# Kernel tuning notes

Measured on AMD Instinct MI355X. Metric: run time of the kernel, lower is better.

Reference implementation:

```python
import jax, jax.numpy as jnp
import numpy as np

N_NODES = 100000


def gcn_conv(x, edge_index, W, b, num_nodes):
    # PyG GCNConv: h = X W; out = D^-1/2 (A+I) D^-1/2 h + b
    h = x @ W
    src, dst = edge_index[0], edge_index[1]
    loop = jnp.arange(num_nodes, dtype=edge_index.dtype)
    src = jnp.concatenate([src, loop])
    dst = jnp.concatenate([dst, loop])
    ew = jnp.ones(src.shape[0], dtype=x.dtype)  # edge_weight=None -> ones
    deg = jax.ops.segment_sum(ew, dst, num_segments=num_nodes)
    dinv = jnp.where(deg > 0, jax.lax.rsqrt(deg), 0.0)
    norm = dinv[src] * ew * dinv[dst]  # [E+N]
    msg = h[src] * norm[:, None]       # gather + scale
    out = jax.ops.segment_sum(msg, dst, num_segments=num_nodes)
    return out + b


def setup_inputs() -> dict:
    key = jax.random.key(0)
    k1, k2, k3, k4 = jax.random.split(key, 4)
    in_c, hid = 128, 128
    x = jax.random.normal(k1, (N_NODES, in_c), dtype=jnp.float32)
    edge_index = jax.random.randint(k2, (2, 1600000), 0, N_NODES, dtype=jnp.int64)
    s = 1.0 / np.sqrt(in_c)
    W1 = jax.random.uniform(k3, (in_c, hid), jnp.float32, -s, s)
    b1 = jnp.zeros((hid,), jnp.float32)
    W2 = jax.random.uniform(k4, (hid, hid), jnp.float32, -s, s)
    b2 = jnp.zeros((hid,), jnp.float32)
    return {"x": x, "edge_index": edge_index, "W1": W1, "b1": b1, "W2": W2, "b2": b2}


def reference(x, edge_index, W1, b1, W2, b2):
    h1 = jax.nn.relu(gcn_conv(x, edge_index, W1, b1, N_NODES))
    h2 = jax.nn.relu(gcn_conv(h1, edge_index, W2, b2, N_NODES))
    return jnp.concatenate([h1, h2], axis=1)  # [N, 2*hidden]
```

## Files before the change

### kernel.cpp

```cpp
#include <hip/hip_runtime.h>
#include <hip/hip_bf16.h>


#define FEAT 128
#define HW 64

typedef __attribute__((ext_vector_type(8))) short short8;
typedef __attribute__((ext_vector_type(4))) float f32x4;

static __device__ inline unsigned pack_bf16(float a, float b) {
    unsigned ua = __float_as_uint(a), ub = __float_as_uint(b);
    ua = (ua + 0x7fff + ((ua >> 16) & 1)) >> 16;
    ub = (ub + 0x7fff + ((ub >> 16) & 1)) >> 16;
    return (ua & 0xffffu) | (ub << 16);
}

static __device__ inline void split2(float x, unsigned short* hi, unsigned short* lo) {
    unsigned u = __float_as_uint(x);
    unsigned uh = (u + 0x7fff + ((u >> 16) & 1)) & 0xffff0000u;
    *hi = (unsigned short)(uh >> 16);
    float lo_f = x - __uint_as_float(uh);
    unsigned ul = __float_as_uint(lo_f);
    *lo = (unsigned short)((ul + 0x7fff + ((ul >> 16) & 1)) >> 16);
}


__global__ void count_edges_kernel(const int* __restrict__ dst, int E,
                                   int* __restrict__ cnt) {
    int e = blockIdx.x * 256 + threadIdx.x;
    if (e < E) atomicAdd(&cnt[dst[e]], 1);
}

__global__ __launch_bounds__(1024) void scan_block_kernel(
    const int* __restrict__ cnt, int* __restrict__ incl,
    int* __restrict__ bsum, float* __restrict__ dinv, int N) {
    __shared__ int s[1024];
    int tid = threadIdx.x;
    int i = blockIdx.x * 1024 + tid;
    int v = (i < N) ? cnt[i] : 0;
    if (i < N) dinv[i] = rsqrtf((float)(v + 1));
    s[tid] = v;
    __syncthreads();
    for (int off = 1; off < 1024; off <<= 1) {
        int add = (tid >= off) ? s[tid - off] : 0;
        __syncthreads();
        s[tid] += add;
        __syncthreads();
    }
    if (i < N) incl[i] = s[tid];
    if (tid == 1023) bsum[blockIdx.x] = s[1023];
}

__global__ __launch_bounds__(128) void scan_bsum_kernel(int* __restrict__ bsum, int NB) {
    __shared__ int s[128];
    int tid = threadIdx.x;
    int v = (tid < NB) ? bsum[tid] : 0;
    s[tid] = v;
    __syncthreads();
    for (int off = 1; off < 128; off <<= 1) {
        int add = (tid >= off) ? s[tid - off] : 0;
        __syncthreads();
        s[tid] += add;
        __syncthreads();
    }
    if (tid < NB) bsum[tid] = s[tid] - v;
}

__global__ void scan_finalize_kernel(const int* __restrict__ incl,
                                     const int* __restrict__ bsum,
                                     int* __restrict__ rowptr, int N) {
    int i = blockIdx.x * 256 + threadIdx.x;
    if (i < N) rowptr[i + 1] = incl[i] + bsum[i >> 10];
    if (i == 0) rowptr[0] = 0;
}

__global__ void fill_csr_kernel(const int* __restrict__ src, const int* __restrict__ dst,
                                int E, const int* __restrict__ rowptr,
                                int* __restrict__ cur, int* __restrict__ csr_src) {
    int e = blockIdx.x * 256 + threadIdx.x;
    if (e < E) {
        int d = dst[e];
        int pos = atomicAdd(&cur[d], 1);
        csr_src[rowptr[d] + pos] = src[e];
    }
}


__global__ void prep_w_kernel(const float* __restrict__ W,
                              unsigned short* __restrict__ wf_hi,
                              unsigned short* __restrict__ wf_lo) {
    int f = blockIdx.x * 256 + threadIdx.x;
    int j = f & 7, lane = (f >> 3) & 63, t = (f >> 9) & 7, ks = f >> 12;
    int k = ks * 32 + (lane >> 4) * 8 + j;
    int n = t * 16 + (lane & 15);
    unsigned short hi, lo;
    split2(W[k * 128 + n], &hi, &lo);
    wf_hi[f] = hi;
    wf_lo[f] = lo;
}


__global__ __launch_bounds__(256) void gemm_mfma_kernel(const float* __restrict__ X, int ldx,
    const unsigned short* __restrict__ wf_hi, const unsigned short* __restrict__ wf_lo,
    unsigned* __restrict__ H, int M) {
    __shared__ unsigned short xs_hi[64 * 128];
    __shared__ unsigned short xs_lo[64 * 128];
    int tid = threadIdx.x;
    int row0 = blockIdx.x * 64;

#pragma unroll
    for (int i = 0; i < 8; ++i) {
        int idx = tid + i * 256;
        int r = idx >> 5, c4 = (idx & 31) * 4;
        int gr = row0 + r;
        float4 v = make_float4(0.f, 0.f, 0.f, 0.f);
        if (gr < M) v = *(const float4*)(X + (size_t)gr * ldx + c4);
        unsigned short h4[4], l4[4];
        split2(v.x, &h4[0], &l4[0]); split2(v.y, &h4[1], &l4[1]);
        split2(v.z, &h4[2], &l4[2]); split2(v.w, &h4[3], &l4[3]);
        int sidx = r * 128 + (c4 ^ ((r & 7) << 3));
        uint2 ph, pl;
        ph.x = (unsigned)h4[0] | ((unsigned)h4[1] << 16);
        ph.y = (unsigned)h4[2] | ((unsigned)h4[3] << 16);
        pl.x = (unsigned)l4[0] | ((unsigned)l4[1] << 16);
        pl.y = (unsigned)l4[2] | ((unsigned)l4[3] << 16);
        *(uint2*)(xs_hi + sidx) = ph;
        *(uint2*)(xs_lo + sidx) = pl;
    }
    __syncthreads();

    int wave = tid >> 6, lane = tid & 63;
    int arow = wave * 16 + (lane & 15);
    int kgrp = (lane >> 4) * 8;

    f32x4 acc[8];
#pragma unroll
    for (int t = 0; t < 8; ++t) acc[t] = (f32x4){0.f, 0.f, 0.f, 0.f};

#pragma unroll
    for (int ks = 0; ks < 4; ++ks) {
        int k0 = ks * 32 + kgrp;
        int aidx = arow * 128 + (k0 ^ ((arow & 7) << 3));
        short8 a_hi = *(const short8*)(xs_hi + aidx);
        short8 a_lo = *(const short8*)(xs_lo + aidx);
        const unsigned short* bp = wf_hi + ((size_t)(ks * 8) * 64 + lane) * 8;
        const unsigned short* bq = wf_lo + ((size_t)(ks * 8) * 64 + lane) * 8;
#pragma unroll
        for (int t = 0; t < 8; ++t) {
            short8 b_hi = *(const short8*)(bp + t * 512);
            short8 b_lo = *(const short8*)(bq + t * 512);
            acc[t] = __builtin_amdgcn_mfma_f32_16x16x32_bf16(a_hi, b_hi, acc[t], 0, 0, 0);
            acc[t] = __builtin_amdgcn_mfma_f32_16x16x32_bf16(a_hi, b_lo, acc[t], 0, 0, 0);
            acc[t] = __builtin_amdgcn_mfma_f32_16x16x32_bf16(a_lo, b_hi, acc[t], 0, 0, 0);
        }
    }

    int rbase = row0 + wave * 16 + (lane >> 4) * 4;
    int c = lane & 15;
#pragma unroll
    for (int r = 0; r < 4; ++r) {
        int gr = rbase + r;
        if (gr < M) {
#pragma unroll
            for (int j = 0; j < 4; ++j) {
                H[(size_t)gr * HW + j * 16 + c] = pack_bf16(acc[2 * j][r], acc[2 * j + 1][r]);
            }
        }
    }
}


__global__ __launch_bounds__(256) void aggregate_kernel(const unsigned* __restrict__ H,
    const float* __restrict__ dinv, const int* __restrict__ rowptr,
    const int* __restrict__ csr_src, const float* __restrict__ bias,
    float* __restrict__ out, int ldo, int coloff, int N) {
    int node = blockIdx.x * 4 + (threadIdx.x >> 6);
    if (node >= N) return;
    int lane = threadIdx.x & 63;
    int f0 = 32 * (lane >> 4) + (lane & 15), f1 = f0 + 16;

    float di = dinv[node];
    float ax, ay;
    {
        unsigned v = H[(size_t)node * HW + lane];
        ax = __uint_as_float(v << 16) * di;
        ay = __uint_as_float(v & 0xffff0000u) * di;
    }

    int e0 = rowptr[node], e1 = rowptr[node + 1];
    int e = e0;
    for (; e + 3 < e1; e += 4) {
        int s0 = csr_src[e + 0], s1 = csr_src[e + 1];
        int s2 = csr_src[e + 2], s3 = csr_src[e + 3];
        float w0 = dinv[s0], w1 = dinv[s1], w2 = dinv[s2], w3 = dinv[s3];
        unsigned v0 = H[(size_t)s0 * HW + lane];
        unsigned v1 = H[(size_t)s1 * HW + lane];
        unsigned v2 = H[(size_t)s2 * HW + lane];
        unsigned v3 = H[(size_t)s3 * HW + lane];
        ax = fmaf(__uint_as_float(v0 << 16), w0, ax);
        ay = fmaf(__uint_as_float(v0 & 0xffff0000u), w0, ay);
        ax = fmaf(__uint_as_float(v1 << 16), w1, ax);
        ay = fmaf(__uint_as_float(v1 & 0xffff0000u), w1, ay);
        ax = fmaf(__uint_as_float(v2 << 16), w2, ax);
        ay = fmaf(__uint_as_float(v2 & 0xffff0000u), w2, ay);
        ax = fmaf(__uint_as_float(v3 << 16), w3, ax);
        ay = fmaf(__uint_as_float(v3 & 0xffff0000u), w3, ay);
    }
    for (; e < e1; ++e) {
        int s = csr_src[e];
        float ws = dinv[s];
        unsigned v = H[(size_t)s * HW + lane];
        ax = fmaf(__uint_as_float(v << 16), ws, ax);
        ay = fmaf(__uint_as_float(v & 0xffff0000u), ws, ay);
    }

    ax = fmaxf(ax * di + bias[f0], 0.f);
    ay = fmaxf(ay * di + bias[f1], 0.f);
    float* orow = out + (size_t)node * ldo + coloff;
    orow[f0] = ax;
    orow[f1] = ay;
}


extern "C" void kernel_launch(void* const* d_in, const int* in_sizes, int n_in,
                              void* d_out, int out_size, void* d_ws, size_t ws_size,
                              hipStream_t stream) {
    const float* x  = (const float*)d_in[0];
    const int*   ei = (const int*)d_in[1];
    const float* W1 = (const float*)d_in[2];
    const float* b1 = (const float*)d_in[3];
    const float* W2 = (const float*)d_in[4];
    const float* b2 = (const float*)d_in[5];
    float* out = (float*)d_out;

    const int N = in_sizes[0] / FEAT;
    const int E = in_sizes[1] / 2;
    const int* srcs = ei;
    const int* dsts = ei + E;

    const int NB = (N + 1023) / 1024;

    char* w = (char*)d_ws;
    unsigned* hb  = (unsigned*)w; w += (size_t)N * HW * sizeof(unsigned);
    float* dinv   = (float*)w; w += (size_t)N * sizeof(float);
    int*   cnt    = (int*)w;   w += (size_t)N * sizeof(int);
    int*   cur    = (int*)w;   w += (size_t)N * sizeof(int);
    int*   rowptr = (int*)w;   w += (size_t)(N + 4) * sizeof(int);
    int*   csr    = (int*)w;   w += (size_t)E * sizeof(int);
    int*   incl   = (int*)w;   w += (size_t)N * sizeof(int);
    int*   bsum   = (int*)w;   w += 128 * sizeof(int);
    unsigned short* wf1_hi = (unsigned short*)w; w += 16384 * sizeof(unsigned short);
    unsigned short* wf1_lo = (unsigned short*)w; w += 16384 * sizeof(unsigned short);
    unsigned short* wf2_hi = (unsigned short*)w; w += 16384 * sizeof(unsigned short);
    unsigned short* wf2_lo = (unsigned short*)w; w += 16384 * sizeof(unsigned short);

    hipMemsetAsync(cnt, 0, (size_t)N * sizeof(int), stream);
    hipMemsetAsync(cur, 0, (size_t)N * sizeof(int), stream);

    int eg = (E + 255) / 256;
    int ng = (N + 255) / 256;
    prep_w_kernel<<<64, 256, 0, stream>>>(W1, wf1_hi, wf1_lo);
    prep_w_kernel<<<64, 256, 0, stream>>>(W2, wf2_hi, wf2_lo);
    count_edges_kernel<<<eg, 256, 0, stream>>>(dsts, E, cnt);
    scan_block_kernel<<<NB, 1024, 0, stream>>>(cnt, incl, bsum, dinv, N);
    scan_bsum_kernel<<<1, 128, 0, stream>>>(bsum, NB);
    scan_finalize_kernel<<<ng, 256, 0, stream>>>(incl, bsum, rowptr, N);
    fill_csr_kernel<<<eg, 256, 0, stream>>>(srcs, dsts, E, rowptr, cur, csr);

    int gg = (N + 63) / 64;
    int ag = (N + 3) / 4;
    gemm_mfma_kernel<<<gg, 256, 0, stream>>>(x, FEAT, wf1_hi, wf1_lo, hb, N);
    aggregate_kernel<<<ag, 256, 0, stream>>>(hb, dinv, rowptr, csr, b1, out, 2 * FEAT, 0, N);
    gemm_mfma_kernel<<<gg, 256, 0, stream>>>(out, 2 * FEAT, wf2_hi, wf2_lo, hb, N);
    aggregate_kernel<<<ag, 256, 0, stream>>>(hb, dinv, rowptr, csr, b2, out, 2 * FEAT, FEAT, N);
}
```

Before: 496.1 us.

## Record edge slot in count pass to drop second atomic CSR fill

```diff
diff --git a/kernel.cpp b/kernel.cpp
--- a/kernel.cpp
+++ b/kernel.cpp
@@ -25,10 +25,10 @@
 }
 
 
-__global__ void count_edges_kernel(const int* __restrict__ dst, int E,
-                                   int* __restrict__ cnt) {
+__global__ void pos_kernel(const int* __restrict__ dst, int E,
+                           int* __restrict__ cnt, int* __restrict__ pos) {
     int e = blockIdx.x * 256 + threadIdx.x;
-    if (e < E) atomicAdd(&cnt[dst[e]], 1);
+    if (e < E) pos[e] = atomicAdd(&cnt[dst[e]], 1);
 }
 
 __global__ __launch_bounds__(1024) void scan_block_kernel(
@@ -74,29 +74,44 @@
     if (i == 0) rowptr[0] = 0;
 }
 
-__global__ void fill_csr_kernel(const int* __restrict__ src, const int* __restrict__ dst,
-                                int E, const int* __restrict__ rowptr,
-                                int* __restrict__ cur, int* __restrict__ csr_src) {
-    int e = blockIdx.x * 256 + threadIdx.x;
-    if (e < E) {
-        int d = dst[e];
-        int pos = atomicAdd(&cur[d], 1);
-        csr_src[rowptr[d] + pos] = src[e];
-    }
-}
-
-
-__global__ void prep_w_kernel(const float* __restrict__ W,
-                              unsigned short* __restrict__ wf_hi,
-                              unsigned short* __restrict__ wf_lo) {
-    int f = blockIdx.x * 256 + threadIdx.x;
+__global__ void scatter_kernel(const int* __restrict__ src, const int* __restrict__ dst,
+                               const int* __restrict__ pos, const int* __restrict__ rowptr,
+                               int* __restrict__ csr_src, int E) {
+    int t = blockIdx.x * 256 + threadIdx.x;
+    int stride = gridDim.x * 256;
+    int E4 = E >> 2;
+    const int4* s4 = (const int4*)src;
+    const int4* d4 = (const int4*)dst;
+    const int4* p4 = (const int4*)pos;
+    for (int i = t; i < E4; i += stride) {
+        int4 d = d4[i], s = s4[i], p = p4[i];
+        csr_src[rowptr[d.x] + p.x] = s.x;
+        csr_src[rowptr[d.y] + p.y] = s.y;
+        csr_src[rowptr[d.z] + p.z] = s.z;
+        csr_src[rowptr[d.w] + p.w] = s.w;
+    }
+    for (int e = E4 * 4 + t; e < E; e += stride) {
+        csr_src[rowptr[dst[e]] + pos[e]] = src[e];
+    }
+}
+
+
+__global__ void prep_w_kernel(const float* __restrict__ W1, const float* __restrict__ W2,
+                              unsigned short* __restrict__ wf1_hi, unsigned short* __restrict__ wf1_lo,
+                              unsigned short* __restrict__ wf2_hi, unsigned short* __restrict__ wf2_lo) {
+    int g = blockIdx.x * 256 + threadIdx.x;
+    int f = g & 16383;
     int j = f & 7, lane = (f >> 3) & 63, t = (f >> 9) & 7, ks = f >> 12;
     int k = ks * 32 + (lane >> 4) * 8 + j;
     int n = t * 16 + (lane & 15);
     unsigned short hi, lo;
-    split2(W[k * 128 + n], &hi, &lo);
-    wf_hi[f] = hi;
-    wf_lo[f] = lo;
+    if (g < 16384) {
+        split2(W1[k * 128 + n], &hi, &lo);
+        wf1_hi[f] = hi; wf1_lo[f] = lo;
+    } else {
+        split2(W2[k * 128 + n], &hi, &lo);
+        wf2_hi[f] = hi; wf2_lo[f] = lo;
+    }
 }
 
 
@@ -189,22 +204,33 @@
 
     int e0 = rowptr[node], e1 = rowptr[node + 1];
     int e = e0;
+    for (; e + 7 < e1; e += 8) {
+        int s[8]; float ws[8]; unsigned v[8];
+#pragma unroll
+        for (int i = 0; i < 8; ++i) s[i] = csr_src[e + i];
+#pragma unroll
+        for (int i = 0; i < 8; ++i) ws[i] = dinv[s[i]];
+#pragma unroll
+        for (int i = 0; i < 8; ++i) v[i] = H[(size_t)s[i] * HW + lane];
+#pragma unroll
+        for (int i = 0; i < 8; ++i) {
+            ax = fmaf(__uint_as_float(v[i] << 16), ws[i], ax);
+            ay = fmaf(__uint_as_float(v[i] & 0xffff0000u), ws[i], ay);
+        }
+    }
     for (; e + 3 < e1; e += 4) {
-        int s0 = csr_src[e + 0], s1 = csr_src[e + 1];
-        int s2 = csr_src[e + 2], s3 = csr_src[e + 3];
-        float w0 = dinv[s0], w1 = dinv[s1], w2 = dinv[s2], w3 = dinv[s3];
-        unsigned v0 = H[(size_t)s0 * HW + lane];
-        unsigned v1 = H[(size_t)s1 * HW + lane];
-        unsigned v2 = H[(size_t)s2 * HW + lane];
-        unsigned v3 = H[(size_t)s3 * HW + lane];
-        ax = fmaf(__uint_as_float(v0 << 16), w0, ax);
-        ay = fmaf(__uint_as_float(v0 & 0xffff0000u), w0, ay);
-        ax = fmaf(__uint_as_float(v1 << 16), w1, ax);
-        ay = fmaf(__uint_as_float(v1 & 0xffff0000u), w1, ay);
-        ax = fmaf(__uint_as_float(v2 << 16), w2, ax);
-        ay = fmaf(__uint_as_float(v2 & 0xffff0000u), w2, ay);
-        ax = fmaf(__uint_as_float(v3 << 16), w3, ax);
-        ay = fmaf(__uint_as_float(v3 & 0xffff0000u), w3, ay);
+        int s[4]; float ws[4]; unsigned v[4];
+#pragma unroll
+        for (int i = 0; i < 4; ++i) s[i] = csr_src[e + i];
+#pragma unroll
+        for (int i = 0; i < 4; ++i) ws[i] = dinv[s[i]];
+#pragma unroll
+        for (int i = 0; i < 4; ++i) v[i] = H[(size_t)s[i] * HW + lane];
+#pragma unroll
+        for (int i = 0; i < 4; ++i) {
+            ax = fmaf(__uint_as_float(v[i] << 16), ws[i], ax);
+            ay = fmaf(__uint_as_float(v[i] & 0xffff0000u), ws[i], ay);
+        }
     }
     for (; e < e1; ++e) {
         int s = csr_src[e];
@@ -244,9 +270,9 @@
     unsigned* hb  = (unsigned*)w; w += (size_t)N * HW * sizeof(unsigned);
     float* dinv   = (float*)w; w += (size_t)N * sizeof(float);
     int*   cnt    = (int*)w;   w += (size_t)N * sizeof(int);
-    int*   cur    = (int*)w;   w += (size_t)N * sizeof(int);
     int*   rowptr = (int*)w;   w += (size_t)(N + 4) * sizeof(int);
     int*   csr    = (int*)w;   w += (size_t)E * sizeof(int);
+    int*   pos    = (int*)w;   w += (size_t)E * sizeof(int);
     int*   incl   = (int*)w;   w += (size_t)N * sizeof(int);
     int*   bsum   = (int*)w;   w += 128 * sizeof(int);
     unsigned short* wf1_hi = (unsigned short*)w; w += 16384 * sizeof(unsigned short);
@@ -255,17 +281,15 @@
     unsigned short* wf2_lo = (unsigned short*)w; w += 16384 * sizeof(unsigned short);
 
     hipMemsetAsync(cnt, 0, (size_t)N * sizeof(int), stream);
-    hipMemsetAsync(cur, 0, (size_t)N * sizeof(int), stream);
 
     int eg = (E + 255) / 256;
     int ng = (N + 255) / 256;
-    prep_w_kernel<<<64, 256, 0, stream>>>(W1, wf1_hi, wf1_lo);
-    prep_w_kernel<<<64, 256, 0, stream>>>(W2, wf2_hi, wf2_lo);
-    count_edges_kernel<<<eg, 256, 0, stream>>>(dsts, E, cnt);
+    prep_w_kernel<<<128, 256, 0, stream>>>(W1, W2, wf1_hi, wf1_lo, wf2_hi, wf2_lo);
+    pos_kernel<<<eg, 256, 0, stream>>>(dsts, E, cnt, pos);
     scan_block_kernel<<<NB, 1024, 0, stream>>>(cnt, incl, bsum, dinv, N);
     scan_bsum_kernel<<<1, 128, 0, stream>>>(bsum, NB);
     scan_finalize_kernel<<<ng, 256, 0, stream>>>(incl, bsum, rowptr, N);
-    fill_csr_kernel<<<eg, 256, 0, stream>>>(srcs, dsts, E, rowptr, cur, csr);
+    scatter_kernel<<<1024, 256, 0, stream>>>(srcs, dsts, pos, rowptr, csr, E);
 
     int gg = (N + 63) / 64;
     int ag = (N + 3) / 4;
```

Measured after the change: 439.8 us. 11.4% less time.
